# Optimization experiments

Measured on AMD Instinct MI355X. Metric: run time of the kernel, lower is better.

## Reference

```python
import jax, jax.numpy as jnp
import numpy as np

H_NODE = 256
H_EDGE = 64
B = 8        # number of graphs
A_PER = 64   # anchors per graph
N_PER = 512  # nodes per graph
INF = 1000000.0
EPS = 1e-8
D_MIN, D_MAX = 0.0, 20.0  # _rbf defaults (gvp-style)


def setup_inputs() -> dict:
    key = jax.random.key(0)
    ks = jax.random.split(key, 16)
    h, he = H_NODE, H_EDGE
    n = lambda k, shp, s=1.0: jax.random.normal(k, shp, jnp.float32) * s
    return {
        "anchor_x": n(ks[0], (B * A_PER, 3), 10.0),
        "node_x": n(ks[1], (B * N_PER, 3), 10.0),
        "anchor_features": n(ks[2], (B * A_PER, h)),
        "node_features": n(ks[3], (B * N_PER, h)),
        "batch": jnp.repeat(jnp.arange(B, dtype=jnp.int32), N_PER),
        "anchor_batch": jnp.repeat(jnp.arange(B, dtype=jnp.int32), A_PER),
        "node_mask": (jax.random.uniform(ks[4], (B * N_PER,)) < 0.9).astype(jnp.float32),
        "Wq": n(ks[5], (h, h), h ** -0.5), "bq": jnp.zeros((h,), jnp.float32),
        "Wkv": n(ks[6], (2 * h, h + he), (h + he) ** -0.5), "bkv": jnp.zeros((2 * h,), jnp.float32),
        "ln1_g": jnp.ones((h,), jnp.float32), "ln1_b": jnp.zeros((h,), jnp.float32),
        "W1": n(ks[7], (2 * h, h), h ** -0.5), "b1": jnp.zeros((2 * h,), jnp.float32),
        "W2": n(ks[8], (2 * h, 2 * h), (2 * h) ** -0.5), "b2": jnp.zeros((2 * h,), jnp.float32),
        "W3": n(ks[9], (h, 2 * h), (2 * h) ** -0.5), "b3": jnp.zeros((h,), jnp.float32),
        "ln2_g": jnp.ones((h,), jnp.float32), "ln2_b": jnp.zeros((h,), jnp.float32),
    }


def _ln(x, g, b, eps=1e-5):
    m = x.mean(-1, keepdims=True)
    v = ((x - m) ** 2).mean(-1, keepdims=True)
    return (x - m) * jax.lax.rsqrt(v + eps) * g + b


def _forward(anchor_x, node_x, anchor_features, node_features, node_mask,
             Wq, bq, Wkv, bkv, ln1_g, ln1_b, W1, b1, W2, b2, W3, b3, ln2_g, ln2_b):
    h, he = H_NODE, H_EDGE
    # equal-sized graphs: reshape global tensors to [B, ., .] (batch ids are repeat(arange(B)))
    q = (anchor_features @ Wq.T + bq).reshape(B, A_PER, h)
    ax = anchor_x.reshape(B, A_PER, 3)
    nx = node_x.reshape(B, N_PER, 3)
    nf = node_features.reshape(B, N_PER, h)
    mask = node_mask.reshape(B, N_PER)

    # pairwise anchor->node distances; original adds scalar eps to the diff vector before the norm
    dist = jnp.linalg.norm(ax[:, :, None, :] - nx[:, None, :, :] + EPS, axis=-1)  # [B,A,N]

    # RBF featurization of dist/10 with D_count = h_edge
    mu = jnp.linspace(D_MIN, D_MAX, he)
    sigma = (D_MAX - D_MIN) / he
    rbf = jnp.exp(-(((dist / 10.0)[..., None] - mu) / sigma) ** 2)  # [B,A,N,he]

    # kv_node(cat([node_feat, rbf])) decomposed: node part computed once per node
    Wkv_n, Wkv_e = Wkv[:, :h], Wkv[:, h:]
    kv_n = nf @ Wkv_n.T + bkv                 # [B,N,2h]
    kv_e = rbf @ Wkv_e.T                      # [B,A,N,2h]
    kv = kv_n[:, None, :, :] + kv_e           # [B,A,N,2h]
    k, v = kv[..., :h], kv[..., h:]

    attn = jnp.einsum('bah,banh->ban', q, k)
    attn = attn * ((mask[:, None, :] - 1.0) * INF)  # faithful to original (multiplicative mask)
    attn = jax.nn.softmax(attn, axis=-1)
    upd = jnp.einsum('ban,banh->bah', attn, v).reshape(B * A_PER, h)

    af = _ln(anchor_features + upd, ln1_g, ln1_b)
    m = jax.nn.relu(af @ W1.T + b1)
    m = jax.nn.relu(m @ W2.T + b2)
    m = m @ W3.T + b3
    return _ln(af + m, ln2_g, ln2_b)


def reference(anchor_x, node_x, anchor_features, node_features, batch, anchor_batch, node_mask,
              Wq, bq, Wkv, bkv, ln1_g, ln1_b, W1, b1, W2, b2, W3, b3, ln2_g, ln2_b):
    # batch / anchor_batch encode equal-sized contiguous graphs; structure is baked into reshapes
    return _forward(anchor_x, node_x, anchor_features, node_features, node_mask,
                    Wq, bq, Wkv, bkv, ln1_g, ln1_b, W1, b1, W2, b2, W3, b3, ln2_g, ln2_b)
```

## Files before the change

kernel.cpp:

```cpp
#include <hip/hip_runtime.h>

#define H    256
#define HE   64
#define NPB  512
#define MU_STEP (20.0f / 63.0f)
#define INV_SIG 3.2f

__device__ __forceinline__ float wave_sum(float v) {
#pragma unroll
    for (int o = 32; o; o >>= 1) v += __shfl_xor(v, o, 64);
    return v;
}
__device__ __forceinline__ float wave_max(float v) {
#pragma unroll
    for (int o = 32; o; o >>= 1) v = fmaxf(v, __shfl_xor(v, o, 64));
    return v;
}
__device__ __forceinline__ float dot4(float4 a, float4 b, float acc) {
    return fmaf(a.x, b.x, fmaf(a.y, b.y, fmaf(a.z, b.z, fmaf(a.w, b.w, acc))));
}

__global__ void __launch_bounds__(1024) fused_all(
    const float* __restrict__ anchor_x, const float* __restrict__ node_x,
    const float* __restrict__ anchor_f, const float* __restrict__ node_f,
    const float* __restrict__ node_mask,
    const float* __restrict__ Wq,  const float* __restrict__ bq,
    const float* __restrict__ Wkv, const float* __restrict__ bkv,
    const float* __restrict__ ln1_g, const float* __restrict__ ln1_b,
    const float* __restrict__ W1, const float* __restrict__ b1,
    const float* __restrict__ W2, const float* __restrict__ b2,
    const float* __restrict__ W3, const float* __restrict__ b3,
    const float* __restrict__ g2,  const float* __restrict__ bb2,
    float* __restrict__ out)
{
    const int bid = blockIdx.x;
    const int b  = bid & 7;
    const int pr = bid >> 3;
    const int aA = b * 64 + 2 * pr;
    const int aB = aA + 1;
    const int t  = threadIdx.x;
    const int wv = t >> 6, l = t & 63;
    const int sub = l >> 4, kc16 = l & 15;

    __shared__ __align__(16) float qWe_s[2][324];
    __shared__ __align__(16) float q_s[2][256];
    __shared__ __align__(16) float af_s[2][256];
    __shared__ __align__(16) float d10_s[2][NPB];
    __shared__ __align__(16) float mf_s[NPB];
    __shared__ __align__(16) float lg_s[2][NPB];
    __shared__ __align__(16) float w_s[2][NPB];
    __shared__ __align__(16) float snf_s[2][256], rj_s[2][64];
    __shared__ __align__(16) float m1_s[2][512], m2_s[2][512];
    __shared__ __align__(16) float red[512], red16[16];
    __shared__ int   idx_s[2][NPB];
    __shared__ int   cnt_s[2];

    if (t < 128) {
        int hh = t >> 6, tt = t & 63;
        ((float4*)af_s[hh])[tt] =
            ((const float4*)anchor_f)[(size_t)(hh ? aB : aA) * 64 + tt];
    }
    if (t < 2) cnt_s[t] = 0;

    if (t < 512) {
        float axA0 = anchor_x[3 * aA], axA1 = anchor_x[3 * aA + 1], axA2 = anchor_x[3 * aA + 2];
        float axB0 = anchor_x[3 * aB], axB1 = anchor_x[3 * aB + 1], axB2 = anchor_x[3 * aB + 2];
        int ng = b * NPB + t;
        float nx0 = node_x[3 * ng], nx1 = node_x[3 * ng + 1], nx2 = node_x[3 * ng + 2];
        float dx = axA0 - nx0 + 1e-8f, dy = axA1 - nx1 + 1e-8f, dz = axA2 - nx2 + 1e-8f;
        d10_s[0][t] = sqrtf(dx * dx + dy * dy + dz * dz) * 0.1f;
        dx = axB0 - nx0 + 1e-8f; dy = axB1 - nx1 + 1e-8f; dz = axB2 - nx2 + 1e-8f;
        d10_s[1][t] = sqrtf(dx * dx + dy * dy + dz * dz) * 0.1f;
        mf_s[t] = (node_mask[ng] - 1.0f) * 1000000.0f;
    }
    __syncthreads();

    {
        float4 aA4[4], aB4[4];
#pragma unroll
        for (int v = 0; v < 4; ++v) {
            aA4[v] = ((const float4*)af_s[0])[16 * v + kc16];
            aB4[v] = ((const float4*)af_s[1])[16 * v + kc16];
        }
#pragma unroll
        for (int pass = 0; pass < 4; ++pass) {
            int m = pass * 64 + wv * 4 + sub;
            const float4* wr = (const float4*)(Wq + (size_t)m * 256);
            float4 w[4];
#pragma unroll
            for (int v = 0; v < 4; ++v) w[v] = wr[16 * v + kc16];
            float aAc = 0.f, aBc = 0.f;
#pragma unroll
            for (int v = 0; v < 4; ++v) {
                aAc = dot4(w[v], aA4[v], aAc);
                aBc = dot4(w[v], aB4[v], aBc);
            }
#pragma unroll
            for (int o = 8; o >= 1; o >>= 1) {
                aAc += __shfl_xor(aAc, o, 64);
                aBc += __shfl_xor(aBc, o, 64);
            }
            if (kc16 == 0) {
                float bv = bq[m];
                q_s[0][m] = aAc + bv;
                q_s[1][m] = aBc + bv;
            }
        }
    }
    __syncthreads();

    {
        int ha = -1, col = 0;
        if (t < 320)                   { ha = 0; col = t; }
        else if (t >= 512 && t < 832)  { ha = 1; col = t - 512; }
        if (ha >= 0) {
            const float* qs = q_s[ha];
            float acc = 0.f;
            for (int o = 0; o < 256; o += 16) {
                float w16[16];
#pragma unroll
                for (int u = 0; u < 16; ++u) w16[u] = Wkv[(size_t)(o + u) * 320 + col];
#pragma unroll
                for (int u = 0; u < 16; ++u) acc = fmaf(w16[u], qs[o + u], acc);
            }
            qWe_s[ha][col] = acc;
        }
    }
    {
        float p = (t < 512) ? q_s[t >> 8][t & 255] * bkv[t & 255] : 0.f;
        p = wave_sum(p);
        if (l == 0) red16[wv] = p;
    }
    __syncthreads();
    const float qbkA = red16[0] + red16[1] + red16[2] + red16[3];
    const float qbkB = red16[4] + red16[5] + red16[6] + red16[7];

    {
        const int g = sub;
        float4 qA4[4], qB4[4];
#pragma unroll
        for (int v = 0; v < 4; ++v) {
            qA4[v] = ((const float4*)qWe_s[0])[4 * kc16 + v];
            qB4[v] = ((const float4*)qWe_s[1])[4 * kc16 + v];
        }
        const float4 qeA4 = ((const float4*)(qWe_s[0] + 256))[kc16];
        const float4 qeB4 = ((const float4*)(qWe_s[1] + 256))[kc16];
        const float mu0 = (4 * kc16 + 0) * MU_STEP, mu1 = (4 * kc16 + 1) * MU_STEP;
        const float mu2 = (4 * kc16 + 2) * MU_STEP, mu3 = (4 * kc16 + 3) * MU_STEP;
        const float4* nfb = (const float4*)(node_f + (size_t)(b * NPB) * 256);

        float4 f[4], fn[4];
        {
            const size_t r0 = (size_t)(wv * 4 + g) * 64 + 4 * kc16;
#pragma unroll
            for (int v = 0; v < 4; ++v) f[v] = nfb[r0 + v];
        }
        for (int it = 0; it < 8; ++it) {
            const int n = it * 64 + wv * 4 + g;
            if (it < 7) {
                const size_t r1 = (size_t)(n + 64) * 64 + 4 * kc16;
#pragma unroll
                for (int v = 0; v < 4; ++v) fn[v] = nfb[r1 + v];
            }
            float sA = 0.f, sB = 0.f;
#pragma unroll
            for (int v = 0; v < 4; ++v) {
                sA = dot4(f[v], qA4[v], sA);
                sB = dot4(f[v], qB4[v], sB);
            }
            const float dA10 = d10_s[0][n], dB10 = d10_s[1][n];
            float u;
            u = (dA10 - mu0) * INV_SIG; sA = fmaf(qeA4.x, __expf(-u * u), sA);
            u = (dA10 - mu1) * INV_SIG; sA = fmaf(qeA4.y, __expf(-u * u), sA);
            u = (dA10 - mu2) * INV_SIG; sA = fmaf(qeA4.z, __expf(-u * u), sA);
            u = (dA10 - mu3) * INV_SIG; sA = fmaf(qeA4.w, __expf(-u * u), sA);
            u = (dB10 - mu0) * INV_SIG; sB = fmaf(qeB4.x, __expf(-u * u), sB);
            u = (dB10 - mu1) * INV_SIG; sB = fmaf(qeB4.y, __expf(-u * u), sB);
            u = (dB10 - mu2) * INV_SIG; sB = fmaf(qeB4.z, __expf(-u * u), sB);
            u = (dB10 - mu3) * INV_SIG; sB = fmaf(qeB4.w, __expf(-u * u), sB);
#pragma unroll
            for (int o = 8; o >= 1; o >>= 1) {
                sA += __shfl_xor(sA, o, 64);
                sB += __shfl_xor(sB, o, 64);
            }
            if (kc16 == 0) {
                lg_s[0][n] = (sA + qbkA) * mf_s[n];
                lg_s[1][n] = (sB + qbkB) * mf_s[n];
            }
#pragma unroll
            for (int v = 0; v < 4; ++v) f[v] = fn[v];
        }
    }
    __syncthreads();

    const int h8 = t >> 9, n9 = t & 511;
    float lg = lg_s[h8][n9];
    {
        float m = wave_max(lg);
        if (l == 0) red16[wv] = m;
    }
    __syncthreads();
    float gmA = red16[0], gmB = red16[8];
#pragma unroll
    for (int i = 1; i < 8; ++i) { gmA = fmaxf(gmA, red16[i]); gmB = fmaxf(gmB, red16[8 + i]); }
    __syncthreads();
    float e = __expf(lg - (h8 ? gmB : gmA));
    w_s[h8][n9] = e;
    {
        float sm = wave_sum(e);
        if (l == 0) red16[wv] = sm;
    }
    __syncthreads();
    float smA = 0.f, smB = 0.f;
#pragma unroll
    for (int i = 0; i < 8; ++i) { smA += red16[i]; smB += red16[8 + i]; }
    const float invA = 1.0f / smA, invB = 1.0f / smB;
    if (e > 0.f) { int p = atomicAdd(&cnt_s[h8], 1); idx_s[h8][p] = n9; }
    __syncthreads();

    if (t < 512) {
        const int hh = t >> 8, col = t & 255;
        const int cnt = cnt_s[hh];
        const float* base = node_f + (size_t)(b * NPB) * 256 + col;
        const int*   idx  = idx_s[hh];
        const float* ws   = w_s[hh];
        float s = 0.f;
        int i = 0;
        for (; i + 8 <= cnt; i += 8) {
            int n0 = idx[i],     n1 = idx[i + 1], n2 = idx[i + 2], n3 = idx[i + 3];
            int n4 = idx[i + 4], n5 = idx[i + 5], n6 = idx[i + 6], n7 = idx[i + 7];
            float f0 = base[(size_t)n0 * 256], f1 = base[(size_t)n1 * 256];
            float f2 = base[(size_t)n2 * 256], f3 = base[(size_t)n3 * 256];
            float f4 = base[(size_t)n4 * 256], f5 = base[(size_t)n5 * 256];
            float f6 = base[(size_t)n6 * 256], f7 = base[(size_t)n7 * 256];
            s = fmaf(ws[n0], f0, s); s = fmaf(ws[n1], f1, s);
            s = fmaf(ws[n2], f2, s); s = fmaf(ws[n3], f3, s);
            s = fmaf(ws[n4], f4, s); s = fmaf(ws[n5], f5, s);
            s = fmaf(ws[n6], f6, s); s = fmaf(ws[n7], f7, s);
        }
        for (; i < cnt; ++i) { int n = idx[i]; s = fmaf(ws[n], base[(size_t)n * 256], s); }
        snf_s[hh][col] = s;
    } else {
        const int tt = t - 512;
        const int ha = tt >> 8, j = tt & 63, g = (tt >> 6) & 3;
        const int cnt = cnt_s[ha];
        const int*   idx = idx_s[ha];
        const float* ws  = w_s[ha];
        const float* ds  = d10_s[ha];
        const float mu = j * MU_STEP;
        float r = 0.f;
        int i = g;
        for (; i + 12 < cnt; i += 16) {
            int n0 = idx[i], n1 = idx[i + 4], n2 = idx[i + 8], n3 = idx[i + 12];
            float u0 = (ds[n0] - mu) * INV_SIG, u1 = (ds[n1] - mu) * INV_SIG;
            float u2 = (ds[n2] - mu) * INV_SIG, u3 = (ds[n3] - mu) * INV_SIG;
            r = fmaf(ws[n0], __expf(-u0 * u0), r);
            r = fmaf(ws[n1], __expf(-u1 * u1), r);
            r = fmaf(ws[n2], __expf(-u2 * u2), r);
            r = fmaf(ws[n3], __expf(-u3 * u3), r);
        }
        for (; i < cnt; i += 4) {
            int n = idx[i];
            float uu = (ds[n] - mu) * INV_SIG;
            r = fmaf(ws[n], __expf(-uu * uu), r);
        }
        red[tt] = r;
    }
    __syncthreads();
    if (t < 128) {
        int ha = t >> 6, j = t & 63;
        rj_s[ha][j] = red[ha * 256 + j] + red[ha * 256 + 64 + j]
                    + red[ha * 256 + 128 + j] + red[ha * 256 + 192 + j];
    }
    __syncthreads();

    {
        float4 sA4[4], sB4[4];
#pragma unroll
        for (int v = 0; v < 4; ++v) {
            sA4[v] = ((const float4*)snf_s[0])[16 * v + kc16];
            sB4[v] = ((const float4*)snf_s[1])[16 * v + kc16];
        }
        const float4 rA4 = ((const float4*)rj_s[0])[kc16];
        const float4 rB4 = ((const float4*)rj_s[1])[kc16];
#pragma unroll
        for (int pass = 0; pass < 4; ++pass) {
            int m = pass * 64 + wv * 4 + sub;
            const float4* wr = (const float4*)(Wkv + (size_t)(256 + m) * 320);
            float4 w[4];
#pragma unroll
            for (int v = 0; v < 4; ++v) w[v] = wr[16 * v + kc16];
            float4 w4 = wr[64 + kc16];
            float aAc = 0.f, aBc = 0.f;
#pragma unroll
            for (int v = 0; v < 4; ++v) {
                aAc = dot4(w[v], sA4[v], aAc);
                aBc = dot4(w[v], sB4[v], aBc);
            }
            aAc = dot4(w4, rA4, aAc);
            aBc = dot4(w4, rB4, aBc);
#pragma unroll
            for (int o = 8; o >= 1; o >>= 1) {
                aAc += __shfl_xor(aAc, o, 64);
                aBc += __shfl_xor(aBc, o, 64);
            }
            if (kc16 == 0) { red[m] = aAc; red[256 + m] = aBc; }
        }
    }
    __syncthreads();

    const int h = (t >> 8) & 1, th = t & 255;
    float x = 0.f;
    if (t < 512)
        x = af_s[h][th] + red[h * 256 + th] * (h ? invB : invA) + bkv[256 + th];
    {
        float s1 = wave_sum(x);
        if (l == 0) red16[wv] = s1;
    }
    __syncthreads();
    float meanA = (red16[0] + red16[1] + red16[2] + red16[3]) * (1.0f / 256.0f);
    float meanB = (red16[4] + red16[5] + red16[6] + red16[7]) * (1.0f / 256.0f);
    __syncthreads();
    float xc = (t < 512) ? (x - (h ? meanB : meanA)) : 0.f;
    {
        float v1 = wave_sum(xc * xc);
        if (l == 0) red16[wv] = v1;
    }
    __syncthreads();
    float varA = (red16[0] + red16[1] + red16[2] + red16[3]) * (1.0f / 256.0f);
    float varB = (red16[4] + red16[5] + red16[6] + red16[7]) * (1.0f / 256.0f);
    __syncthreads();
    if (t < 512)
        af_s[h][th] = xc * rsqrtf((h ? varB : varA) + 1e-5f) * ln1_g[th] + ln1_b[th];
    __syncthreads();

    {
        float4 aA4[4], aB4[4];
#pragma unroll
        for (int v = 0; v < 4; ++v) {
            aA4[v] = ((const float4*)af_s[0])[16 * v + kc16];
            aB4[v] = ((const float4*)af_s[1])[16 * v + kc16];
        }
#pragma unroll
        for (int pass = 0; pass < 8; ++pass) {
            int m = pass * 64 + wv * 4 + sub;
            const float4* wr = (const float4*)(W1 + (size_t)m * 256);
            float4 w[4];
#pragma unroll
            for (int v = 0; v < 4; ++v) w[v] = wr[16 * v + kc16];
            float aAc = 0.f, aBc = 0.f;
#pragma unroll
            for (int v = 0; v < 4; ++v) {
                aAc = dot4(w[v], aA4[v], aAc);
                aBc = dot4(w[v], aB4[v], aBc);
            }
#pragma unroll
            for (int o = 8; o >= 1; o >>= 1) {
                aAc += __shfl_xor(aAc, o, 64);
                aBc += __shfl_xor(aBc, o, 64);
            }
            if (kc16 == 0) {
                float bv = b1[m];
                m1_s[0][m] = fmaxf(aAc + bv, 0.f);
                m1_s[1][m] = fmaxf(aBc + bv, 0.f);
            }
        }
    }
    __syncthreads();

#pragma unroll
    for (int pass = 0; pass < 8; ++pass) {
        int m = pass * 64 + wv * 4 + sub;
        const float4* wr = (const float4*)(W2 + (size_t)m * 512);
        const float4* mA = (const float4*)m1_s[0];
        const float4* mB = (const float4*)m1_s[1];
        float aAc = 0.f, aBc = 0.f;
#pragma unroll
        for (int u = 0; u < 2; ++u) {
            float4 w[4], xA[4], xB[4];
#pragma unroll
            for (int v = 0; v < 4; ++v) {
                int c4 = (u * 4 + v) * 16 + kc16;
                w[v] = wr[c4]; xA[v] = mA[c4]; xB[v] = mB[c4];
            }
#pragma unroll
            for (int v = 0; v < 4; ++v) {
                aAc = dot4(w[v], xA[v], aAc);
                aBc = dot4(w[v], xB[v], aBc);
            }
        }
#pragma unroll
        for (int o = 8; o >= 1; o >>= 1) {
            aAc += __shfl_xor(aAc, o, 64);
            aBc += __shfl_xor(aBc, o, 64);
        }
        if (kc16 == 0) {
            float bv = b2[m];
            m2_s[0][m] = fmaxf(aAc + bv, 0.f);
            m2_s[1][m] = fmaxf(aBc + bv, 0.f);
        }
    }
    __syncthreads();

#pragma unroll
    for (int pass = 0; pass < 4; ++pass) {
        int m = pass * 64 + wv * 4 + sub;
        const float4* wr = (const float4*)(W3 + (size_t)m * 512);
        const float4* mA = (const float4*)m2_s[0];
        const float4* mB = (const float4*)m2_s[1];
        float aAc = 0.f, aBc = 0.f;
#pragma unroll
        for (int u = 0; u < 2; ++u) {
            float4 w[4], xA[4], xB[4];
#pragma unroll
            for (int v = 0; v < 4; ++v) {
                int c4 = (u * 4 + v) * 16 + kc16;
                w[v] = wr[c4]; xA[v] = mA[c4]; xB[v] = mB[c4];
            }
#pragma unroll
            for (int v = 0; v < 4; ++v) {
                aAc = dot4(w[v], xA[v], aAc);
                aBc = dot4(w[v], xB[v], aBc);
            }
        }
#pragma unroll
        for (int o = 8; o >= 1; o >>= 1) {
            aAc += __shfl_xor(aAc, o, 64);
            aBc += __shfl_xor(aBc, o, 64);
        }
        if (kc16 == 0) {
            float bv = b3[m];
            red[m]       = aAc + bv;
            red[256 + m] = aBc + bv;
        }
    }
    __syncthreads();

    float y = 0.f;
    if (t < 512) y = red[h * 256 + th] + af_s[h][th];
    {
        float s1 = wave_sum(y);
        if (l == 0) red16[wv] = s1;
    }
    __syncthreads();
    float mnA = (red16[0] + red16[1] + red16[2] + red16[3]) * (1.0f / 256.0f);
    float mnB = (red16[4] + red16[5] + red16[6] + red16[7]) * (1.0f / 256.0f);
    __syncthreads();
    float yc = (t < 512) ? (y - (h ? mnB : mnA)) : 0.f;
    {
        float v1 = wave_sum(yc * yc);
        if (l == 0) red16[wv] = v1;
    }
    __syncthreads();
    float vrA = (red16[0] + red16[1] + red16[2] + red16[3]) * (1.0f / 256.0f);
    float vrB = (red16[4] + red16[5] + red16[6] + red16[7]) * (1.0f / 256.0f);
    if (t < 512) {
        int aOut = h ? aB : aA;
        out[(size_t)aOut * 256 + th] =
            yc * rsqrtf((h ? vrB : vrA) + 1e-5f) * g2[th] + bb2[th];
    }
}

extern "C" void kernel_launch(void* const* d_in, const int* in_sizes, int n_in,
                              void* d_out, int out_size, void* d_ws, size_t ws_size,
                              hipStream_t stream)
{
    const float* anchor_x  = (const float*)d_in[0];
    const float* node_x    = (const float*)d_in[1];
    const float* anchor_f  = (const float*)d_in[2];
    const float* node_f    = (const float*)d_in[3];
    const float* node_mask = (const float*)d_in[6];
    const float* Wq        = (const float*)d_in[7];
    const float* bq        = (const float*)d_in[8];
    const float* Wkv       = (const float*)d_in[9];
    const float* bkv       = (const float*)d_in[10];
    const float* ln1_g     = (const float*)d_in[11];
    const float* ln1_b     = (const float*)d_in[12];
    const float* W1        = (const float*)d_in[13];
    const float* b1        = (const float*)d_in[14];
    const float* W2        = (const float*)d_in[15];
    const float* b2        = (const float*)d_in[16];
    const float* W3        = (const float*)d_in[17];
    const float* b3        = (const float*)d_in[18];
    const float* ln2_g     = (const float*)d_in[19];
    const float* ln2_b     = (const float*)d_in[20];

    fused_all<<<256, 1024, 0, stream>>>(anchor_x, node_x, anchor_f, node_f,
                                        node_mask, Wq, bq, Wkv, bkv,
                                        ln1_g, ln1_b, W1, b1, W2, b2, W3, b3,
                                        ln2_g, ln2_b, (float*)d_out);
}
```

Measured before the change: 148.4 us.

## Dense float4 node aggregation, one-pass layernorm stats, fewer barriers

Drops the atomic compaction of nonzero-weight nodes. Aggregation now streams every node's features densely with float4 loads and register prefetch, and partial sums are combined through shared memory. The q projection reads anchor features straight from global, which removes a barrier. Both layernorms now get mean and sum of squares in one reduction pass, and the softmax uses separate reduction slots, which removes several __syncthreads. The trade-off is loading masked nodes (about 10%) and a less numerically stable E[x²]−mean² variance.

```diff
diff --git a/kernel.cpp b/kernel.cpp
--- a/kernel.cpp
+++ b/kernel.cpp
@@ -51,17 +51,48 @@
     __shared__ __align__(16) float w_s[2][NPB];
     __shared__ __align__(16) float snf_s[2][256], rj_s[2][64];
     __shared__ __align__(16) float m1_s[2][512], m2_s[2][512];
-    __shared__ __align__(16) float red[512], red16[16];
-    __shared__ int   idx_s[2][NPB];
-    __shared__ int   cnt_s[2];
+    __shared__ __align__(16) float red[512], red16[32];
+    __shared__ __align__(16) float4 s4_s[512];
 
     if (t < 128) {
         int hh = t >> 6, tt = t & 63;
         ((float4*)af_s[hh])[tt] =
             ((const float4*)anchor_f)[(size_t)(hh ? aB : aA) * 64 + tt];
     }
-    if (t < 2) cnt_s[t] = 0;
-
+    {
+        const float4* afA = (const float4*)anchor_f + (size_t)aA * 64;
+        const float4* afB = (const float4*)anchor_f + (size_t)aB * 64;
+        float4 aA4[4], aB4[4];
+#pragma unroll
+        for (int v = 0; v < 4; ++v) {
+            aA4[v] = afA[16 * v + kc16];
+            aB4[v] = afB[16 * v + kc16];
+        }
+#pragma unroll
+        for (int pass = 0; pass < 4; ++pass) {
+            int m = pass * 64 + wv * 4 + sub;
+            const float4* wr = (const float4*)(Wq + (size_t)m * 256);
+            float4 w[4];
+#pragma unroll
+            for (int v = 0; v < 4; ++v) w[v] = wr[16 * v + kc16];
+            float aAc = 0.f, aBc = 0.f;
+#pragma unroll
+            for (int v = 0; v < 4; ++v) {
+                aAc = dot4(w[v], aA4[v], aAc);
+                aBc = dot4(w[v], aB4[v], aBc);
+            }
+#pragma unroll
+            for (int o = 8; o >= 1; o >>= 1) {
+                aAc += __shfl_xor(aAc, o, 64);
+                aBc += __shfl_xor(aBc, o, 64);
+            }
+            if (kc16 == 0) {
+                float bv = bq[m];
+                q_s[0][m] = aAc + bv;
+                q_s[1][m] = aBc + bv;
+            }
+        }
+    }
     if (t < 512) {
         float axA0 = anchor_x[3 * aA], axA1 = anchor_x[3 * aA + 1], axA2 = anchor_x[3 * aA + 2];
         float axB0 = anchor_x[3 * aB], axB1 = anchor_x[3 * aB + 1], axB2 = anchor_x[3 * aB + 2];
@@ -76,40 +107,6 @@
     __syncthreads();
 
     {
-        float4 aA4[4], aB4[4];
-#pragma unroll
-        for (int v = 0; v < 4; ++v) {
-            aA4[v] = ((const float4*)af_s[0])[16 * v + kc16];
-            aB4[v] = ((const float4*)af_s[1])[16 * v + kc16];
-        }
-#pragma unroll
-        for (int pass = 0; pass < 4; ++pass) {
-            int m = pass * 64 + wv * 4 + sub;
-            const float4* wr = (const float4*)(Wq + (size_t)m * 256);
-            float4 w[4];
-#pragma unroll
-            for (int v = 0; v < 4; ++v) w[v] = wr[16 * v + kc16];
-            float aAc = 0.f, aBc = 0.f;
-#pragma unroll
-            for (int v = 0; v < 4; ++v) {
-                aAc = dot4(w[v], aA4[v], aAc);
-                aBc = dot4(w[v], aB4[v], aBc);
-            }
-#pragma unroll
-            for (int o = 8; o >= 1; o >>= 1) {
-                aAc += __shfl_xor(aAc, o, 64);
-                aBc += __shfl_xor(aBc, o, 64);
-            }
-            if (kc16 == 0) {
-                float bv = bq[m];
-                q_s[0][m] = aAc + bv;
-                q_s[1][m] = aBc + bv;
-            }
-        }
-    }
-    __syncthreads();
-
-    {
         int ha = -1, col = 0;
         if (t < 320)                   { ha = 0; col = t; }
         else if (t >= 512 && t < 832)  { ha = 1; col = t - 512; }
@@ -203,72 +200,80 @@
     float gmA = red16[0], gmB = red16[8];
 #pragma unroll
     for (int i = 1; i < 8; ++i) { gmA = fmaxf(gmA, red16[i]); gmB = fmaxf(gmB, red16[8 + i]); }
-    __syncthreads();
     float e = __expf(lg - (h8 ? gmB : gmA));
     w_s[h8][n9] = e;
     {
         float sm = wave_sum(e);
-        if (l == 0) red16[wv] = sm;
+        if (l == 0) red16[16 + wv] = sm;
     }
     __syncthreads();
     float smA = 0.f, smB = 0.f;
 #pragma unroll
-    for (int i = 0; i < 8; ++i) { smA += red16[i]; smB += red16[8 + i]; }
+    for (int i = 0; i < 8; ++i) { smA += red16[16 + i]; smB += red16[24 + i]; }
     const float invA = 1.0f / smA, invB = 1.0f / smB;
-    if (e > 0.f) { int p = atomicAdd(&cnt_s[h8], 1); idx_s[h8][p] = n9; }
+
+    if (t < 512) {
+        const int hh = t >> 8, r8 = t & 255;
+        const int cg = r8 >> 2, sub4 = r8 & 3;
+        const float4* nfb = (const float4*)(node_f + (size_t)(b * NPB) * 256);
+        const float* ws = w_s[hh];
+        float4 acc = make_float4(0.f, 0.f, 0.f, 0.f);
+        float4 f[4], g[4];
+#pragma unroll
+        for (int v = 0; v < 4; ++v)
+            f[v] = nfb[(size_t)(sub4 + 4 * v) * 64 + cg];
+        for (int it = 0; it < 32; ++it) {
+            const int n0 = it * 16 + sub4;
+            if (it < 31) {
+                const int n1 = n0 + 16;
+#pragma unroll
+                for (int v = 0; v < 4; ++v)
+                    g[v] = nfb[(size_t)(n1 + 4 * v) * 64 + cg];
+            }
+#pragma unroll
+            for (int v = 0; v < 4; ++v) {
+                const float w = ws[n0 + 4 * v];
+                acc.x = fmaf(w, f[v].x, acc.x);
+                acc.y = fmaf(w, f[v].y, acc.y);
+                acc.z = fmaf(w, f[v].z, acc.z);
+                acc.w = fmaf(w, f[v].w, acc.w);
+            }
+#pragma unroll
+            for (int v = 0; v < 4; ++v) f[v] = g[v];
+        }
+        s4_s[t] = acc;
+    } else {
+        const int tt = t - 512;
+        const int ha = tt >> 8, j = tt & 63, g4 = (tt >> 6) & 3;
+        const float* ws = w_s[ha];
+        const float* ds = d10_s[ha];
+        const float mu = j * MU_STEP;
+        float r0 = 0.f, r1 = 0.f, r2 = 0.f, r3 = 0.f;
+        for (int i = g4; i < 512; i += 16) {
+            float u0 = (ds[i]      - mu) * INV_SIG;
+            float u1 = (ds[i + 4]  - mu) * INV_SIG;
+            float u2 = (ds[i + 8]  - mu) * INV_SIG;
+            float u3 = (ds[i + 12] - mu) * INV_SIG;
+            r0 = fmaf(ws[i],      __expf(-u0 * u0), r0);
+            r1 = fmaf(ws[i + 4],  __expf(-u1 * u1), r1);
+            r2 = fmaf(ws[i + 8],  __expf(-u2 * u2), r2);
+            r3 = fmaf(ws[i + 12], __expf(-u3 * u3), r3);
+        }
+        red[tt] = (r0 + r1) + (r2 + r3);
+    }
     __syncthreads();
 
     if (t < 512) {
         const int hh = t >> 8, col = t & 255;
-        const int cnt = cnt_s[hh];
-        const float* base = node_f + (size_t)(b * NPB) * 256 + col;
-        const int*   idx  = idx_s[hh];
-        const float* ws   = w_s[hh];
-        float s = 0.f;
-        int i = 0;
-        for (; i + 8 <= cnt; i += 8) {
-            int n0 = idx[i],     n1 = idx[i + 1], n2 = idx[i + 2], n3 = idx[i + 3];
-            int n4 = idx[i + 4], n5 = idx[i + 5], n6 = idx[i + 6], n7 = idx[i + 7];
-            float f0 = base[(size_t)n0 * 256], f1 = base[(size_t)n1 * 256];
-            float f2 = base[(size_t)n2 * 256], f3 = base[(size_t)n3 * 256];
-            float f4 = base[(size_t)n4 * 256], f5 = base[(size_t)n5 * 256];
-            float f6 = base[(size_t)n6 * 256], f7 = base[(size_t)n7 * 256];
-            s = fmaf(ws[n0], f0, s); s = fmaf(ws[n1], f1, s);
-            s = fmaf(ws[n2], f2, s); s = fmaf(ws[n3], f3, s);
-            s = fmaf(ws[n4], f4, s); s = fmaf(ws[n5], f5, s);
-            s = fmaf(ws[n6], f6, s); s = fmaf(ws[n7], f7, s);
-        }
-        for (; i < cnt; ++i) { int n = idx[i]; s = fmaf(ws[n], base[(size_t)n * 256], s); }
-        snf_s[hh][col] = s;
-    } else {
+        const int cg = col >> 2, cm = col & 3;
+        const float* p0 = (const float*)&s4_s[hh * 256 + cg * 4 + 0];
+        const float* p1 = (const float*)&s4_s[hh * 256 + cg * 4 + 1];
+        const float* p2 = (const float*)&s4_s[hh * 256 + cg * 4 + 2];
+        const float* p3 = (const float*)&s4_s[hh * 256 + cg * 4 + 3];
+        snf_s[hh][col] = (p0[cm] + p1[cm]) + (p2[cm] + p3[cm]);
+    } else if (t < 640) {
         const int tt = t - 512;
-        const int ha = tt >> 8, j = tt & 63, g = (tt >> 6) & 3;
-        const int cnt = cnt_s[ha];
-        const int*   idx = idx_s[ha];
-        const float* ws  = w_s[ha];
-        const float* ds  = d10_s[ha];
-        const float mu = j * MU_STEP;
-        float r = 0.f;
-        int i = g;
-        for (; i + 12 < cnt; i += 16) {
-            int n0 = idx[i], n1 = idx[i + 4], n2 = idx[i + 8], n3 = idx[i + 12];
-            float u0 = (ds[n0] - mu) * INV_SIG, u1 = (ds[n1] - mu) * INV_SIG;
-            float u2 = (ds[n2] - mu) * INV_SIG, u3 = (ds[n3] - mu) * INV_SIG;
-            r = fmaf(ws[n0], __expf(-u0 * u0), r);
-            r = fmaf(ws[n1], __expf(-u1 * u1), r);
-            r = fmaf(ws[n2], __expf(-u2 * u2), r);
-            r = fmaf(ws[n3], __expf(-u3 * u3), r);
-        }
-        for (; i < cnt; i += 4) {
-            int n = idx[i];
-            float uu = (ds[n] - mu) * INV_SIG;
-            r = fmaf(ws[n], __expf(-uu * uu), r);
-        }
-        red[tt] = r;
-    }
-    __syncthreads();
-    if (t < 128) {
-        int ha = t >> 6, j = t & 63;
+        const int ha = tt >> 6, j = tt & 63;
         rj_s[ha][j] = red[ha * 256 + j] + red[ha * 256 + 64 + j]
                     + red[ha * 256 + 128 + j] + red[ha * 256 + 192 + j];
     }
@@ -315,23 +320,21 @@
         x = af_s[h][th] + red[h * 256 + th] * (h ? invB : invA) + bkv[256 + th];
     {
         float s1 = wave_sum(x);
-        if (l == 0) red16[wv] = s1;
-    }
-    __syncthreads();
-    float meanA = (red16[0] + red16[1] + red16[2] + red16[3]) * (1.0f / 256.0f);
-    float meanB = (red16[4] + red16[5] + red16[6] + red16[7]) * (1.0f / 256.0f);
-    __syncthreads();
-    float xc = (t < 512) ? (x - (h ? meanB : meanA)) : 0.f;
-    {
-        float v1 = wave_sum(xc * xc);
-        if (l == 0) red16[wv] = v1;
-    }
-    __syncthreads();
-    float varA = (red16[0] + red16[1] + red16[2] + red16[3]) * (1.0f / 256.0f);
-    float varB = (red16[4] + red16[5] + red16[6] + red16[7]) * (1.0f / 256.0f);
-    __syncthreads();
-    if (t < 512)
-        af_s[h][th] = xc * rsqrtf((h ? varB : varA) + 1e-5f) * ln1_g[th] + ln1_b[th];
+        float s2 = wave_sum(x * x);
+        if (l == 0) { red16[wv] = s1; red16[16 + wv] = s2; }
+    }
+    __syncthreads();
+    {
+        float meanA = (red16[0] + red16[1] + red16[2] + red16[3]) * (1.0f / 256.0f);
+        float meanB = (red16[4] + red16[5] + red16[6] + red16[7]) * (1.0f / 256.0f);
+        float sqA   = (red16[16] + red16[17] + red16[18] + red16[19]) * (1.0f / 256.0f);
+        float sqB   = (red16[20] + red16[21] + red16[22] + red16[23]) * (1.0f / 256.0f);
+        float varA = sqA - meanA * meanA, varB = sqB - meanB * meanB;
+        if (t < 512) {
+            float xc = x - (h ? meanB : meanA);
+            af_s[h][th] = xc * rsqrtf((h ? varB : varA) + 1e-5f) * ln1_g[th] + ln1_b[th];
+        }
+    }
     __syncthreads();
 
     {
@@ -440,24 +443,22 @@
     if (t < 512) y = red[h * 256 + th] + af_s[h][th];
     {
         float s1 = wave_sum(y);
-        if (l == 0) red16[wv] = s1;
-    }
-    __syncthreads();
-    float mnA = (red16[0] + red16[1] + red16[2] + red16[3]) * (1.0f / 256.0f);
-    float mnB = (red16[4] + red16[5] + red16[6] + red16[7]) * (1.0f / 256.0f);
-    __syncthreads();
-    float yc = (t < 512) ? (y - (h ? mnB : mnA)) : 0.f;
-    {
-        float v1 = wave_sum(yc * yc);
-        if (l == 0) red16[wv] = v1;
-    }
-    __syncthreads();
-    float vrA = (red16[0] + red16[1] + red16[2] + red16[3]) * (1.0f / 256.0f);
-    float vrB = (red16[4] + red16[5] + red16[6] + red16[7]) * (1.0f / 256.0f);
-    if (t < 512) {
-        int aOut = h ? aB : aA;
-        out[(size_t)aOut * 256 + th] =
-            yc * rsqrtf((h ? vrB : vrA) + 1e-5f) * g2[th] + bb2[th];
+        float s2 = wave_sum(y * y);
+        if (l == 0) { red16[wv] = s1; red16[16 + wv] = s2; }
+    }
+    __syncthreads();
+    {
+        float mnA = (red16[0] + red16[1] + red16[2] + red16[3]) * (1.0f / 256.0f);
+        float mnB = (red16[4] + red16[5] + red16[6] + red16[7]) * (1.0f / 256.0f);
+        float sqA = (red16[16] + red16[17] + red16[18] + red16[19]) * (1.0f / 256.0f);
+        float sqB = (red16[20] + red16[21] + red16[22] + red16[23]) * (1.0f / 256.0f);
+        float vrA = sqA - mnA * mnA, vrB = sqB - mnB * mnB;
+        if (t < 512) {
+            float yc = y - (h ? mnB : mnA);
+            int aOut = h ? aB : aA;
+            out[(size_t)aOut * 256 + th] =
+                yc * rsqrtf((h ? vrB : vrA) + 1e-5f) * g2[th] + bb2[th];
+        }
     }
 }
 
```

Measured after the change: 173.7 us. +17.1%, slower.
